# Optimization experiments

Measured on AMD Instinct MI355X. Metric: run time of the kernel, lower is better.

## Reference

```python
import jax, jax.numpy as jnp
import numpy as np

# ---- static hash-grid config (matches tcnn HashGrid in __init__) ----
L = 16            # n_levels
T = 1 << 19       # hashmap size per level
BASE = 16
MAXR = 4096
GEO = 15
SCALE = np.exp((np.log(MAXR) - np.log(BASE)) / (L - 1))
RES = np.floor(BASE * SCALE ** np.arange(L)).astype(np.int64)  # per-level resolution
PRIMES = np.array([1, 2654435761, 805459861], dtype=np.uint32)
CORNERS = np.array([[(i >> 2) & 1, (i >> 1) & 1, i & 1] for i in range(8)], dtype=np.float32)  # [8,3]


@jax.custom_vjp
def trunc_exp(x):
    return jnp.exp(x)

def _te_fwd(x):
    return jnp.exp(x), x

def _te_bwd(x, g):
    return (g * jnp.exp(jnp.minimum(x, 15.0)),)

trunc_exp.defvjp(_te_fwd, _te_bwd)


def hash_encode(x, tables):
    """Multi-res hash grid. x: [N,3] in [0,1]; tables: [L,T,2] -> [N, 2*L]."""
    x = jnp.clip(x, 0.0, 1.0)
    feats = []
    for l in range(L):  # fixed small loop over levels
        res = float(RES[l])
        pos = x * res                      # [N,3]
        p0 = jnp.floor(pos)
        f = pos - p0                       # trilinear fractions
        idx = (p0[:, None, :] + CORNERS[None]).astype(jnp.uint32)  # [N,8,3]
        h = (idx[..., 0] * PRIMES[0]) ^ (idx[..., 1] * PRIMES[1]) ^ (idx[..., 2] * PRIMES[2])
        h = (h % np.uint32(T)).astype(jnp.int32)                   # [N,8]
        w = jnp.prod(jnp.where(CORNERS[None] > 0, f[:, None, :], 1.0 - f[:, None, :]), axis=-1)  # [N,8]
        feats.append(jnp.sum(tables[l][h] * w[..., None], axis=1))  # [N,2]
    return jnp.concatenate(feats, axis=-1)  # [N,32]


def sh_deg4(d):
    """Spherical harmonics degree 4 (16 comps) on unit directions d: [N,3]."""
    x, y, z = d[..., 0], d[..., 1], d[..., 2]
    x2, y2, z2 = x * x, y * y, z * z
    xy, yz, xz = x * y, y * z, x * z
    return jnp.stack([
        jnp.full_like(x, 0.28209479177387814),
        -0.48860251190291987 * y, 0.48860251190291987 * z, -0.48860251190291987 * x,
        1.0925484305920792 * xy, -1.0925484305920792 * yz,
        0.94617469575755997 * z2 - 0.31539156525252005,
        -1.0925484305920792 * xz, 0.54627421529603959 * (x2 - y2),
        -0.5900435899266435 * y * (3 * x2 - y2), 2.890611442640554 * xy * z,
        -0.4570457994644658 * y * (4 * z2 - x2 - y2),
        0.3731763325901154 * z * (2 * z2 - 3 * x2 - 3 * y2),
        -0.4570457994644658 * x * (4 * z2 - x2 - y2),
        1.445305721320277 * z * (x2 - y2),
        -0.5900435899266435 * x * (x2 - 3 * y2),
    ], axis=-1)


def setup_inputs() -> dict:
    key = jax.random.key(0)
    ks = jax.random.split(key, 12)
    R, N = 8192, 524288
    rays_o = jax.random.uniform(ks[0], (R, 3), minval=-0.4, maxval=0.4, dtype=jnp.float32)
    d = jax.random.normal(ks[1], (R, 3), dtype=jnp.float32)
    rays_d = d / jnp.linalg.norm(d, axis=-1, keepdims=True)
    ray_indices = jnp.sort(jax.random.randint(ks[2], (N,), 0, R)).astype(jnp.int32)
    t_starts = jax.random.uniform(ks[3], (N,), dtype=jnp.float32) * 0.25
    t_ends = t_starts + jax.random.uniform(ks[4], (N,), dtype=jnp.float32) * 0.02 + 1e-3
    hash_tables = jax.random.uniform(ks[5], (L, T, 2), minval=-1e-4, maxval=1e-4, dtype=jnp.float32)
    base_w0 = jax.random.normal(ks[6], (32, 64), dtype=jnp.float32) * (1.0 / np.sqrt(32))
    base_w1 = jax.random.normal(ks[7], (64, 16), dtype=jnp.float32) * (1.0 / np.sqrt(64))
    head_w0 = jax.random.normal(ks[8], (31, 64), dtype=jnp.float32) * (1.0 / np.sqrt(31))
    head_w1 = jax.random.normal(ks[9], (64, 64), dtype=jnp.float32) * (1.0 / np.sqrt(64))
    head_w2 = jax.random.normal(ks[10], (64, 3), dtype=jnp.float32) * (1.0 / np.sqrt(64))
    aabb = jnp.array([-1., -1., -1., 1., 1., 1.], dtype=jnp.float32)
    return dict(t_starts=t_starts, t_ends=t_ends, rays_o=rays_o, rays_d=rays_d,
                ray_indices=ray_indices, hash_tables=hash_tables,
                base_w0=base_w0, base_w1=base_w1,
                head_w0=head_w0, head_w1=head_w1, head_w2=head_w2, aabb=aabb)


def reference(t_starts, t_ends, rays_o, rays_d, ray_indices, hash_tables,
              base_w0, base_w1, head_w0, head_w1, head_w2, aabb):
    n_rays = rays_o.shape[0]
    aabb_min, aabb_max = aabb[:3], aabb[3:]
    # gather per-sample origins/dirs (irregular gather)
    t_origins = rays_o[ray_indices]
    t_dirs = rays_d[ray_indices]
    tmid = (t_starts + t_ends) * 0.5
    positions = t_origins + t_dirs * tmid[:, None]
    # query_density
    xn = (positions - aabb_min) / (aabb_max - aabb_min + 1e-5)
    selector = jnp.all((xn > 0.0) & (xn < 1.0), axis=-1)
    enc = hash_encode(xn, hash_tables)                   # [N,32]
    h = jax.nn.relu(enc @ base_w0) @ base_w1             # [N,16]
    sigmas = trunc_exp(h[:, 0] - 1.0) * selector         # [N]
    embedding = h[:, 1:]                                 # [N,15]
    # query_rgb: dir=(dir+1)/2 then SH enc maps back to [-1,1] => SH(t_dirs)
    hh = jnp.concatenate([sh_deg4(t_dirs), embedding], axis=-1)  # [N,31]
    rgbs = jax.nn.sigmoid(jax.nn.relu(jax.nn.relu(hh @ head_w0) @ head_w1) @ head_w2)  # [N,3]
    # render_weight_from_density: segment-wise exclusive transmittance
    s = sigmas * (t_ends - t_starts)
    excl = jnp.cumsum(s) - s                              # global exclusive cumsum
    offsets = jax.ops.segment_min(excl, ray_indices, num_segments=n_rays)  # value at each segment start
    trans = jnp.exp(-(excl - offsets[ray_indices]))
    alphas = 1.0 - jnp.exp(-s)
    weights = trans * alphas
    # accumulate_along_rays (segment_sum scatter)
    colors = jax.ops.segment_sum(weights[:, None] * rgbs, ray_indices, num_segments=n_rays)
    opacities = jax.ops.segment_sum(weights, ray_indices, num_segments=n_rays)[:, None]
    depths = jax.ops.segment_sum(weights * tmid, ray_indices, num_segments=n_rays)[:, None]
    depths = depths / jnp.maximum(opacities, jnp.finfo(jnp.float32).eps)  # expected_depths
    return colors, opacities, depths
```

## Files before the change

kernel.cpp:

```cpp
#include <hip/hip_runtime.h>
#include <math.h>

#define NLEV 16
#define TBL  (1u << 19)
#define TMASK (TBL - 1u)

typedef _Float16 half2v  __attribute__((ext_vector_type(2)));
typedef _Float16 half4   __attribute__((ext_vector_type(4)));
typedef _Float16 half8   __attribute__((ext_vector_type(8)));
typedef float    floatx4 __attribute__((ext_vector_type(4)));
typedef unsigned int uint2v __attribute__((ext_vector_type(2)));
typedef unsigned int uint4v __attribute__((ext_vector_type(4)));

struct ResParams { float resf[NLEV]; };

__device__ __forceinline__ float sigmoidf(float x) {
    return 1.0f / (1.0f + __expf(-x));
}

__device__ __forceinline__ float2 unpack_h2(unsigned u) {
    union { unsigned u; half2v h; } c; c.u = u;
    return make_float2((float)c.h[0], (float)c.h[1]);
}

__device__ __forceinline__ int swz64(int row, int col) {
    return row * 64 + ((((col >> 3) ^ (row & 7)) << 3) | (col & 7));
}
__device__ __forceinline__ int swz64_blk(int row, int blk) {
    return row * 64 + ((blk ^ (row & 7)) << 3);
}
__device__ __forceinline__ int swz16(int row, int col) {
    return row * 64 + ((((col >> 3) ^ (row & 7)) << 3) | (col & 7));
}
__device__ __forceinline__ int swz16_blk(int row, int blk) {
    return row * 64 + ((blk ^ (row & 7)) << 3);
}

__global__ __launch_bounds__(256) void k_cvt(
    const float* __restrict__ src, _Float16* __restrict__ dst, int n4)
{
    const int i = blockIdx.x * 256 + threadIdx.x;
    if (i >= n4) return;
    const float4 v = ((const float4*)src)[i];
    half4 o; o[0] = (_Float16)v.x; o[1] = (_Float16)v.y;
    o[2] = (_Float16)v.z; o[3] = (_Float16)v.w;
    ((half4*)dst)[i] = o;
}

struct SampPos { float x0, x1, x2; };

__device__ __forceinline__ SampPos load_pos(
    int i, const float* __restrict__ t_starts, const float* __restrict__ t_ends,
    const float* __restrict__ rays_o, const float* __restrict__ rays_d,
    const int* __restrict__ ray_indices,
    float a0, float a1, float a2, float ib0, float ib1, float ib2)
{
    const int   ri = ray_indices[i];
    const float tmid = 0.5f * (t_starts[i] + t_ends[i]);
    const float xn0 = (rays_o[ri*3+0] + rays_d[ri*3+0]*tmid - a0) * ib0;
    const float xn1 = (rays_o[ri*3+1] + rays_d[ri*3+1]*tmid - a1) * ib1;
    const float xn2 = (rays_o[ri*3+2] + rays_d[ri*3+2]*tmid - a2) * ib2;
    SampPos p;
    p.x0 = fminf(fmaxf(xn0, 0.f), 1.f);
    p.x1 = fminf(fmaxf(xn1, 0.f), 1.f);
    p.x2 = fminf(fmaxf(xn2, 0.f), 1.f);
    return p;
}

__global__ __launch_bounds__(256) void k_hash1(
    const float* __restrict__ t_starts, const float* __restrict__ t_ends,
    const float* __restrict__ rays_o,   const float* __restrict__ rays_d,
    const int*   __restrict__ ray_indices,
    const _Float16* __restrict__ tabh,
    const float* __restrict__ aabb,
    _Float16* __restrict__ encG, int n, ResParams rp)
{
    const int i = blockIdx.x * 256 + threadIdx.x;
    if (i >= n) return;

    const float a0 = aabb[0], a1 = aabb[1], a2 = aabb[2];
    const float ib0 = 1.f / (aabb[3] - a0 + 1e-5f);
    const float ib1 = 1.f / (aabb[4] - a1 + 1e-5f);
    const float ib2 = 1.f / (aabb[5] - a2 + 1e-5f);

    const SampPos A = load_pos(i, t_starts, t_ends, rays_o, rays_d, ray_indices,
                               a0, a1, a2, ib0, ib1, ib2);

    union { _Float16 h[32]; uint4v q[4]; } ev;

    #pragma unroll
    for (int l = 0; l < NLEV; ++l) {
        const float resf = rp.resf[l];
        const _Float16* __restrict__ tab = tabh + (size_t)l * (size_t)(TBL * 2u);

        const float p0 = A.x0*resf, p1 = A.x1*resf, p2 = A.x2*resf;
        const float fl0 = floorf(p0), fl1 = floorf(p1), fl2 = floorf(p2);
        const float f0 = p0-fl0, f1 = p1-fl1, f2 = p2-fl2;
        const unsigned i0 = (unsigned)fl0, i1 = (unsigned)fl1, i2 = (unsigned)fl2;
        const unsigned hy0 = i1 * 2654435761u, hy1 = hy0 + 2654435761u;
        const unsigned hz0 = i2 * 805459861u,  hz1 = hz0 + 805459861u;
        const float g0 = 1.f-f0, g1 = 1.f-f1, g2 = 1.f-f2;
        const unsigned ryz[4] = { hy0^hz0, hy0^hz1, hy1^hz0, hy1^hz1 };
        const float    wyz[4] = { g1*g2,   g1*f2,   f1*g2,   f1*f2 };

        unsigned v0[4], v1[4];
        if (!(i0 & 1u)) {
            #pragma unroll
            for (int c = 0; c < 4; ++c) {
                const unsigned lo = (i0 ^ ryz[c]) & TMASK;
                const uint2v p = *(const uint2v*)(tab + (size_t)(lo & ~1u) * 2u);
                const unsigned sw = lo & 1u;
                v0[c] = sw ? p.y : p.x;
                v1[c] = sw ? p.x : p.y;
            }
        } else {
            #pragma unroll
            for (int c = 0; c < 4; ++c) {
                const unsigned lo = (i0        ^ ryz[c]) & TMASK;
                const unsigned hi = ((i0 + 1u) ^ ryz[c]) & TMASK;
                v0[c] = *(const unsigned*)(tab + (size_t)lo * 2u);
                v1[c] = *(const unsigned*)(tab + (size_t)hi * 2u);
            }
        }

        float e0 = 0.f, e1 = 0.f;
        #pragma unroll
        for (int c = 0; c < 4; ++c) {
            const float wlo = g0 * wyz[c], whi = f0 * wyz[c];
            const float2 t0 = unpack_h2(v0[c]), t1 = unpack_h2(v1[c]);
            e0 += wlo * t0.x + whi * t1.x;
            e1 += wlo * t0.y + whi * t1.y;
        }
        ev.h[2*l]   = (_Float16)(e0 * 1024.f);
        ev.h[2*l+1] = (_Float16)(e1 * 1024.f);
    }

    uint4v* dst = (uint4v*)(encG + (size_t)i * 32);
    #pragma unroll
    for (int q = 0; q < 4; ++q) __builtin_nontemporal_store(ev.q[q], dst + q);
}

__global__ __launch_bounds__(256) void k_bounds(
    const int* __restrict__ ray_indices, int* __restrict__ se, int n)
{
    const int i = blockIdx.x * 256 + threadIdx.x;
    if (i >= n) return;
    const int r = ray_indices[i];
    if (i == 0 || ray_indices[i-1] != r) se[2*r]     = i;
    if (i == n-1 || ray_indices[i+1] != r) se[2*r+1] = i + 1;
}

__global__ __launch_bounds__(256) void k_mlp(
    const float* __restrict__ t_starts, const float* __restrict__ t_ends,
    const float* __restrict__ rays_o,   const float* __restrict__ rays_d,
    const int*   __restrict__ ray_indices,
    const float* __restrict__ bw0,
    const float* __restrict__ bw1,
    const float* __restrict__ hw0,
    const float* __restrict__ hw1,
    const float* __restrict__ hw2,
    const float* __restrict__ aabb,
    const _Float16* __restrict__ encG,
    float4* __restrict__ srgb, int n)
{
    __shared__ _Float16 sT  [4][2048];
    __shared__ _Float16 sSH [256 * 16];
    __shared__ _Float16 sHB [256 * 16];
    __shared__ _Float16 sW0T[64 * 40];
    __shared__ _Float16 sW1T[64 * 64];
    __shared__ _Float16 sBW0T[64 * 32];
    __shared__ _Float16 sBW1T[16 * 64];
    __shared__ float    sDT [256];

    const int t     = threadIdx.x;
    const int gbase = blockIdx.x * 256;

    {
        const int s  = gbase + t;
        const int ri = ray_indices[s];
        const float ts = t_starts[s], te = t_ends[s];
        const float tmid = 0.5f * (ts + te);
        const float ox = rays_o[ri*3+0], oy = rays_o[ri*3+1], oz = rays_o[ri*3+2];
        const float dx = rays_d[ri*3+0], dy = rays_d[ri*3+1], dz = rays_d[ri*3+2];
        const float a0 = aabb[0], a1 = aabb[1], a2c = aabb[2];
        const float b0 = aabb[3], b1 = aabb[4], b2c = aabb[5];
        const float xn0 = (ox + dx*tmid - a0) / (b0 - a0 + 1e-5f);
        const float xn1 = (oy + dy*tmid - a1) / (b1 - a1 + 1e-5f);
        const float xn2 = (oz + dz*tmid - a2c) / (b2c - a2c + 1e-5f);
        const bool sel = (xn0 > 0.f) && (xn0 < 1.f) && (xn1 > 0.f) && (xn1 < 1.f)
                      && (xn2 > 0.f) && (xn2 < 1.f);
        sDT[t] = sel ? (te - ts) : 0.f;

        const float x = dx, y = dy, z = dz;
        const float x2 = x*x, y2 = y*y, z2 = z*z;
        const float xy = x*y, yz = y*z, xz = x*z;
        float shv[16];
        shv[0]  = 0.28209479177387814f;
        shv[1]  = -0.48860251190291987f * y;
        shv[2]  = 0.48860251190291987f * z;
        shv[3]  = -0.48860251190291987f * x;
        shv[4]  = 1.0925484305920792f * xy;
        shv[5]  = -1.0925484305920792f * yz;
        shv[6]  = 0.94617469575756f * z2 - 0.31539156525252005f;
        shv[7]  = -1.0925484305920792f * xz;
        shv[8]  = 0.5462742152960396f * (x2 - y2);
        shv[9]  = -0.5900435899266435f * y * (3.f*x2 - y2);
        shv[10] = 2.890611442640554f * xy * z;
        shv[11] = -0.4570457994644658f * y * (4.f*z2 - x2 - y2);
        shv[12] = 0.3731763325901154f * z * (2.f*z2 - 3.f*x2 - 3.f*y2);
        shv[13] = -0.4570457994644658f * x * (4.f*z2 - x2 - y2);
        shv[14] = 1.445305721320277f * z * (x2 - y2);
        shv[15] = -0.5900435899266435f * x * (x2 - 3.f*y2);
        #pragma unroll
        for (int k4 = 0; k4 < 4; ++k4) {
            half4 p;
            #pragma unroll
            for (int j = 0; j < 4; ++j) p[j] = (_Float16)shv[k4*4 + j];
            *(half4*)&sSH[t*16 + k4*4] = p;
        }
    }
    {
        const int nidx = t & 63, g = t >> 6;
        #pragma unroll
        for (int i2 = 0; i2 < 8; ++i2) {
            const int k = g*8 + i2;
            const float v = (k < 31) ? hw0[k*64 + nidx] : 0.f;
            sW0T[nidx*40 + k] = (_Float16)v;
        }
        #pragma unroll
        for (int i2 = 0; i2 < 16; ++i2) {
            const int k = g*16 + i2;
            sW1T[swz64(nidx, k)] = (_Float16)hw1[k*64 + nidx];
        }
        #pragma unroll
        for (int i2 = 0; i2 < 8; ++i2) {
            const int k = g*8 + i2;
            sBW0T[nidx*32 + k] = (_Float16)bw0[k*64 + nidx];
        }
    }
    {
        const int nidx = t & 15, g = t >> 4;
        #pragma unroll
        for (int i2 = 0; i2 < 4; ++i2) {
            const int k = g*4 + i2;
            sBW1T[swz16(nidx, k)] = (_Float16)bw1[k*16 + nidx];
        }
    }

    const int lane = t & 63, w = t >> 6;
    const int nn = lane & 15, quad = lane >> 4;
    _Float16* T0 = &sT[w][0];
    _Float16* T1 = &sT[w][1024];

    half8 BH2[2];
    #pragma unroll
    for (int ks = 0; ks < 2; ++ks)
        #pragma unroll
        for (int j = 0; j < 8; ++j) {
            const int k = ks*32 + quad*8 + j;
            BH2[ks][j] = (nn < 3) ? (_Float16)hw2[k*3 + nn] : (_Float16)0.f;
        }

    __syncthreads();

    const int rbase = w * 64;

    #pragma unroll
    for (int p = 0; p < 2; ++p) {
        const int s0 = rbase + p*32;
        const int s1 = s0 + 16;
        const int d0 = s0 + quad*4;
        const int d1 = s1 + quad*4;

        half8 bE0 = *(const half8*)(encG + (size_t)(gbase + s0 + nn)*32 + quad*8);
        half8 bE1 = *(const half8*)(encG + (size_t)(gbase + s1 + nn)*32 + quad*8);
        #pragma unroll
        for (int ct = 0; ct < 4; ++ct) {
            half8 aW = *(const half8*)&sBW0T[(ct*16 + nn)*32 + quad*8];
            floatx4 a0 = {0.f,0.f,0.f,0.f}, a1 = {0.f,0.f,0.f,0.f};
            a0 = __builtin_amdgcn_mfma_f32_16x16x32_f16(aW, bE0, a0, 0, 0, 0);
            a1 = __builtin_amdgcn_mfma_f32_16x16x32_f16(aW, bE1, a1, 0, 0, 0);
            half4 p0, p1;
            #pragma unroll
            for (int r2 = 0; r2 < 4; ++r2) {
                p0[r2] = (_Float16)fmaxf(a0[r2], 0.f);
                p1[r2] = (_Float16)fmaxf(a1[r2], 0.f);
            }
            *(half4*)&T0[swz16(nn, ct*16 + quad*4)] = p0;
            *(half4*)&T1[swz16(nn, ct*16 + quad*4)] = p1;
        }

        float sig0[4], sig1[4];
        {
            half8 b20 = *(const half8*)&sBW1T[swz16_blk(nn, quad)];
            half8 b21 = *(const half8*)&sBW1T[swz16_blk(nn, 4 + quad)];
            half8 a200 = *(const half8*)&T0[swz16_blk(nn, quad)];
            half8 a201 = *(const half8*)&T0[swz16_blk(nn, 4 + quad)];
            half8 a210 = *(const half8*)&T1[swz16_blk(nn, quad)];
            half8 a211 = *(const half8*)&T1[swz16_blk(nn, 4 + quad)];
            floatx4 c0 = {0.f,0.f,0.f,0.f}, c1 = {0.f,0.f,0.f,0.f};
            c0 = __builtin_amdgcn_mfma_f32_16x16x32_f16(a200, b20, c0, 0, 0, 0);
            c1 = __builtin_amdgcn_mfma_f32_16x16x32_f16(a210, b20, c1, 0, 0, 0);
            c0 = __builtin_amdgcn_mfma_f32_16x16x32_f16(a201, b21, c0, 0, 0, 0);
            c1 = __builtin_amdgcn_mfma_f32_16x16x32_f16(a211, b21, c1, 0, 0, 0);
            #pragma unroll
            for (int r2 = 0; r2 < 4; ++r2) {
                const float h0v = c0[r2] * (1.f / 1024.f);
                const float h1v = c1[r2] * (1.f / 1024.f);
                const float b0v = __shfl(h0v, lane & 0x30, 64);
                const float b1v = __shfl(h1v, lane & 0x30, 64);
                sig0[r2] = __expf(b0v - 1.f) * sDT[d0 + r2];
                sig1[r2] = __expf(b1v - 1.f) * sDT[d1 + r2];
                if (nn == 0) {
                    sHB[(d0 + r2)*16 + 15] = (_Float16)0.f;
                    sHB[(d1 + r2)*16 + 15] = (_Float16)0.f;
                } else {
                    sHB[(d0 + r2)*16 + (nn - 1)] = (_Float16)h0v;
                    sHB[(d1 + r2)*16 + (nn - 1)] = (_Float16)h1v;
                }
            }
        }

        half8 sh0 = *(const half8*)&sSH[(s0 + nn)*16 + (quad & 1)*8];
        half8 hb0 = *(const half8*)&sHB[(s0 + nn)*16 + (quad & 1)*8];
        half8 sh1 = *(const half8*)&sSH[(s1 + nn)*16 + (quad & 1)*8];
        half8 hb1 = *(const half8*)&sHB[(s1 + nn)*16 + (quad & 1)*8];
        half8 f30 = (quad < 2) ? sh0 : hb0;
        half8 f31 = (quad < 2) ? sh1 : hb1;
        #pragma unroll
        for (int ct = 0; ct < 4; ++ct) {
            half8 aW = *(const half8*)&sW0T[(ct*16 + nn)*40 + quad*8];
            floatx4 a0 = {0.f,0.f,0.f,0.f}, a1 = {0.f,0.f,0.f,0.f};
            a0 = __builtin_amdgcn_mfma_f32_16x16x32_f16(aW, f30, a0, 0, 0, 0);
            a1 = __builtin_amdgcn_mfma_f32_16x16x32_f16(aW, f31, a1, 0, 0, 0);
            half4 p0, p1;
            #pragma unroll
            for (int r2 = 0; r2 < 4; ++r2) {
                p0[r2] = (_Float16)fmaxf(a0[r2], 0.f);
                p1[r2] = (_Float16)fmaxf(a1[r2], 0.f);
            }
            *(half4*)&T0[swz16(nn, ct*16 + quad*4)] = p0;
            *(half4*)&T1[swz16(nn, ct*16 + quad*4)] = p1;
        }

        half8 af00 = *(const half8*)&T0[swz16_blk(nn, quad)];
        half8 af01 = *(const half8*)&T0[swz16_blk(nn, 4 + quad)];
        half8 af10 = *(const half8*)&T1[swz16_blk(nn, quad)];
        half8 af11 = *(const half8*)&T1[swz16_blk(nn, 4 + quad)];
        #pragma unroll
        for (int ct = 0; ct < 4; ++ct) {
            half8 aW0 = *(const half8*)&sW1T[swz64_blk(ct*16 + nn, quad)];
            half8 aW1 = *(const half8*)&sW1T[swz64_blk(ct*16 + nn, 4 + quad)];
            floatx4 a0 = {0.f,0.f,0.f,0.f}, a1 = {0.f,0.f,0.f,0.f};
            a0 = __builtin_amdgcn_mfma_f32_16x16x32_f16(aW0, af00, a0, 0, 0, 0);
            a1 = __builtin_amdgcn_mfma_f32_16x16x32_f16(aW0, af10, a1, 0, 0, 0);
            a0 = __builtin_amdgcn_mfma_f32_16x16x32_f16(aW1, af01, a0, 0, 0, 0);
            a1 = __builtin_amdgcn_mfma_f32_16x16x32_f16(aW1, af11, a1, 0, 0, 0);
            half4 p0, p1;
            #pragma unroll
            for (int r2 = 0; r2 < 4; ++r2) {
                p0[r2] = (_Float16)fmaxf(a0[r2], 0.f);
                p1[r2] = (_Float16)fmaxf(a1[r2], 0.f);
            }
            *(half4*)&T0[swz16(nn, ct*16 + quad*4)] = p0;
            *(half4*)&T1[swz16(nn, ct*16 + quad*4)] = p1;
        }

        {
            half8 a500 = *(const half8*)&T0[swz16_blk(nn, quad)];
            half8 a501 = *(const half8*)&T0[swz16_blk(nn, 4 + quad)];
            half8 a510 = *(const half8*)&T1[swz16_blk(nn, quad)];
            half8 a511 = *(const half8*)&T1[swz16_blk(nn, 4 + quad)];
            floatx4 c0 = {0.f,0.f,0.f,0.f}, c1 = {0.f,0.f,0.f,0.f};
            c0 = __builtin_amdgcn_mfma_f32_16x16x32_f16(a500, BH2[0], c0, 0, 0, 0);
            c1 = __builtin_amdgcn_mfma_f32_16x16x32_f16(a510, BH2[0], c1, 0, 0, 0);
            c0 = __builtin_amdgcn_mfma_f32_16x16x32_f16(a501, BH2[1], c0, 0, 0, 0);
            c1 = __builtin_amdgcn_mfma_f32_16x16x32_f16(a511, BH2[1], c1, 0, 0, 0);
            #pragma unroll
            for (int r2 = 0; r2 < 4; ++r2) {
                float* bp0 = (float*)&srgb[gbase + d0 + r2];
                float* bp1 = (float*)&srgb[gbase + d1 + r2];
                if (nn < 3) {
                    bp0[1 + nn] = sigmoidf(c0[r2]);
                    bp1[1 + nn] = sigmoidf(c1[r2]);
                } else if (nn == 3) {
                    bp0[0] = sig0[r2];
                    bp1[0] = sig1[r2];
                }
            }
        }
    }
}

__global__ __launch_bounds__(256) void k_render(
    const float* __restrict__ t_starts, const float* __restrict__ t_ends,
    const int*   __restrict__ se,
    const float4* __restrict__ srgb,
    float* __restrict__ out, int n_rays)
{
    const int wid  = (blockIdx.x * 256 + threadIdx.x) >> 6;
    const int lane = threadIdx.x & 63;
    if (wid >= n_rays) return;
    const int r = wid;

    const int start = se[2*r];
    const int end   = se[2*r + 1];

    float S = 0.f, cr = 0.f, cg = 0.f, cb = 0.f, op = 0.f, dw = 0.f;
    for (int j0 = start; j0 < end; j0 += 64) {
        const int j = j0 + lane;
        float s = 0.f, R = 0.f, G = 0.f, B = 0.f, tm = 0.f;
        if (j < end) {
            const float4 v = srgb[j];
            s = v.x; R = v.y; G = v.z; B = v.w;
            tm = 0.5f * (t_starts[j] + t_ends[j]);
        }
        float incl = s;
        #pragma unroll
        for (int off = 1; off < 64; off <<= 1) {
            const float tv = __shfl_up(incl, off, 64);
            if (lane >= off) incl += tv;
        }
        const float excl  = incl - s;
        const float trans = __expf(-(S + excl));
        const float alpha = 1.f - __expf(-s);
        const float wgt   = trans * alpha;
        cr += wgt * R; cg += wgt * G; cb += wgt * B;
        op += wgt;     dw += wgt * tm;
        S += __shfl(incl, 63, 64);
    }
    #pragma unroll
    for (int off = 1; off < 64; off <<= 1) {
        cr += __shfl_xor(cr, off, 64);
        cg += __shfl_xor(cg, off, 64);
        cb += __shfl_xor(cb, off, 64);
        op += __shfl_xor(op, off, 64);
        dw += __shfl_xor(dw, off, 64);
    }
    if (lane == 0) {
        out[r*3 + 0] = cr;
        out[r*3 + 1] = cg;
        out[r*3 + 2] = cb;
        out[n_rays*3 + r] = op;
        out[n_rays*4 + r] = dw / fmaxf(op, 1.1920929e-7f);
    }
}

extern "C" void kernel_launch(void* const* d_in, const int* in_sizes, int n_in,
                              void* d_out, int out_size, void* d_ws, size_t ws_size,
                              hipStream_t stream)
{
    const float* t_starts    = (const float*)d_in[0];
    const float* t_ends      = (const float*)d_in[1];
    const float* rays_o      = (const float*)d_in[2];
    const float* rays_d      = (const float*)d_in[3];
    const int*   ray_indices = (const int*)  d_in[4];
    const float* tables      = (const float*)d_in[5];
    const float* bw0         = (const float*)d_in[6];
    const float* bw1         = (const float*)d_in[7];
    const float* hw0         = (const float*)d_in[8];
    const float* hw1         = (const float*)d_in[9];
    const float* hw2         = (const float*)d_in[10];
    const float* aabb        = (const float*)d_in[11];

    const int n      = in_sizes[0];
    const int n_rays = in_sizes[2] / 3;
    const int tbl_n  = in_sizes[5];

    float* out = (float*)d_out;
    char*  ws  = (char*)d_ws;

    const size_t tabh_bytes = (size_t)tbl_n * 2;
    const size_t enc_bytes  = (size_t)n * 64;
    const size_t srgb_bytes = (size_t)n * 16;

    ResParams rp;
    const double scale = exp((log(4096.0) - log(16.0)) / 15.0);
    for (int l = 0; l < NLEV; ++l)
        rp.resf[l] = (float)floor(16.0 * pow(scale, (double)l));

    _Float16* tabh = (_Float16*)ws;
    _Float16* encG = (_Float16*)(ws + tabh_bytes);
    float4*   srgb = (float4*)(ws + tabh_bytes + enc_bytes);
    int*      se   = (int*)(ws + tabh_bytes + enc_bytes + srgb_bytes);

    const int n4 = tbl_n / 4;
    k_cvt<<<(n4 + 255)/256, 256, 0, stream>>>(tables, tabh, n4);

    hipMemsetAsync(se, 0, (size_t)n_rays * 2 * sizeof(int), stream);
    k_bounds<<<(n + 255)/256, 256, 0, stream>>>(ray_indices, se, n);

    k_hash1<<<(n + 255)/256, 256, 0, stream>>>(
        t_starts, t_ends, rays_o, rays_d, ray_indices, tabh, aabb, encG, n, rp);

    k_mlp<<<(n + 255)/256, 256, 0, stream>>>(
        t_starts, t_ends, rays_o, rays_d, ray_indices, bw0, bw1, hw0, hw1, hw2,
        aabb, encG, srgb, n);

    k_render<<<(n_rays*64 + 255)/256, 256, 0, stream>>>(
        t_starts, t_ends, se, srgb, out, n_rays);
}
```

Baseline: 312.9 us.

## Fuse hash-grid encoding into MLP kernel, computing features directly in MFMA fragments

Removes the separate hash-encoding kernel and its fp16 feature buffer in global memory. Each lane now computes the four hash levels matching its quad for the four sample rows it feeds to the first MFMA, writing results straight into the B-operand registers. This drops a global write and read of 64 bytes per sample and one launch. In exchange, the MLP kernel carries the gather latency and extra register pressure, which may lower occupancy, and the ray position is recomputed per lane.

```diff
diff --git a/kernel.cpp b/kernel.cpp
--- a/kernel.cpp
+++ b/kernel.cpp
@@ -47,99 +47,6 @@
     ((half4*)dst)[i] = o;
 }
 
-struct SampPos { float x0, x1, x2; };
-
-__device__ __forceinline__ SampPos load_pos(
-    int i, const float* __restrict__ t_starts, const float* __restrict__ t_ends,
-    const float* __restrict__ rays_o, const float* __restrict__ rays_d,
-    const int* __restrict__ ray_indices,
-    float a0, float a1, float a2, float ib0, float ib1, float ib2)
-{
-    const int   ri = ray_indices[i];
-    const float tmid = 0.5f * (t_starts[i] + t_ends[i]);
-    const float xn0 = (rays_o[ri*3+0] + rays_d[ri*3+0]*tmid - a0) * ib0;
-    const float xn1 = (rays_o[ri*3+1] + rays_d[ri*3+1]*tmid - a1) * ib1;
-    const float xn2 = (rays_o[ri*3+2] + rays_d[ri*3+2]*tmid - a2) * ib2;
-    SampPos p;
-    p.x0 = fminf(fmaxf(xn0, 0.f), 1.f);
-    p.x1 = fminf(fmaxf(xn1, 0.f), 1.f);
-    p.x2 = fminf(fmaxf(xn2, 0.f), 1.f);
-    return p;
-}
-
-__global__ __launch_bounds__(256) void k_hash1(
-    const float* __restrict__ t_starts, const float* __restrict__ t_ends,
-    const float* __restrict__ rays_o,   const float* __restrict__ rays_d,
-    const int*   __restrict__ ray_indices,
-    const _Float16* __restrict__ tabh,
-    const float* __restrict__ aabb,
-    _Float16* __restrict__ encG, int n, ResParams rp)
-{
-    const int i = blockIdx.x * 256 + threadIdx.x;
-    if (i >= n) return;
-
-    const float a0 = aabb[0], a1 = aabb[1], a2 = aabb[2];
-    const float ib0 = 1.f / (aabb[3] - a0 + 1e-5f);
-    const float ib1 = 1.f / (aabb[4] - a1 + 1e-5f);
-    const float ib2 = 1.f / (aabb[5] - a2 + 1e-5f);
-
-    const SampPos A = load_pos(i, t_starts, t_ends, rays_o, rays_d, ray_indices,
-                               a0, a1, a2, ib0, ib1, ib2);
-
-    union { _Float16 h[32]; uint4v q[4]; } ev;
-
-    #pragma unroll
-    for (int l = 0; l < NLEV; ++l) {
-        const float resf = rp.resf[l];
-        const _Float16* __restrict__ tab = tabh + (size_t)l * (size_t)(TBL * 2u);
-
-        const float p0 = A.x0*resf, p1 = A.x1*resf, p2 = A.x2*resf;
-        const float fl0 = floorf(p0), fl1 = floorf(p1), fl2 = floorf(p2);
-        const float f0 = p0-fl0, f1 = p1-fl1, f2 = p2-fl2;
-        const unsigned i0 = (unsigned)fl0, i1 = (unsigned)fl1, i2 = (unsigned)fl2;
-        const unsigned hy0 = i1 * 2654435761u, hy1 = hy0 + 2654435761u;
-        const unsigned hz0 = i2 * 805459861u,  hz1 = hz0 + 805459861u;
-        const float g0 = 1.f-f0, g1 = 1.f-f1, g2 = 1.f-f2;
-        const unsigned ryz[4] = { hy0^hz0, hy0^hz1, hy1^hz0, hy1^hz1 };
-        const float    wyz[4] = { g1*g2,   g1*f2,   f1*g2,   f1*f2 };
-
-        unsigned v0[4], v1[4];
-        if (!(i0 & 1u)) {
-            #pragma unroll
-            for (int c = 0; c < 4; ++c) {
-                const unsigned lo = (i0 ^ ryz[c]) & TMASK;
-                const uint2v p = *(const uint2v*)(tab + (size_t)(lo & ~1u) * 2u);
-                const unsigned sw = lo & 1u;
-                v0[c] = sw ? p.y : p.x;
-                v1[c] = sw ? p.x : p.y;
-            }
-        } else {
-            #pragma unroll
-            for (int c = 0; c < 4; ++c) {
-                const unsigned lo = (i0        ^ ryz[c]) & TMASK;
-                const unsigned hi = ((i0 + 1u) ^ ryz[c]) & TMASK;
-                v0[c] = *(const unsigned*)(tab + (size_t)lo * 2u);
-                v1[c] = *(const unsigned*)(tab + (size_t)hi * 2u);
-            }
-        }
-
-        float e0 = 0.f, e1 = 0.f;
-        #pragma unroll
-        for (int c = 0; c < 4; ++c) {
-            const float wlo = g0 * wyz[c], whi = f0 * wyz[c];
-            const float2 t0 = unpack_h2(v0[c]), t1 = unpack_h2(v1[c]);
-            e0 += wlo * t0.x + whi * t1.x;
-            e1 += wlo * t0.y + whi * t1.y;
-        }
-        ev.h[2*l]   = (_Float16)(e0 * 1024.f);
-        ev.h[2*l+1] = (_Float16)(e1 * 1024.f);
-    }
-
-    uint4v* dst = (uint4v*)(encG + (size_t)i * 32);
-    #pragma unroll
-    for (int q = 0; q < 4; ++q) __builtin_nontemporal_store(ev.q[q], dst + q);
-}
-
 __global__ __launch_bounds__(256) void k_bounds(
     const int* __restrict__ ray_indices, int* __restrict__ se, int n)
 {
@@ -150,18 +57,18 @@
     if (i == n-1 || ray_indices[i+1] != r) se[2*r+1] = i + 1;
 }
 
-__global__ __launch_bounds__(256) void k_mlp(
+__global__ __launch_bounds__(256) void k_fused(
     const float* __restrict__ t_starts, const float* __restrict__ t_ends,
     const float* __restrict__ rays_o,   const float* __restrict__ rays_d,
     const int*   __restrict__ ray_indices,
+    const _Float16* __restrict__ tabh,
     const float* __restrict__ bw0,
     const float* __restrict__ bw1,
     const float* __restrict__ hw0,
     const float* __restrict__ hw1,
     const float* __restrict__ hw2,
     const float* __restrict__ aabb,
-    const _Float16* __restrict__ encG,
-    float4* __restrict__ srgb, int n)
+    float4* __restrict__ srgb, int n, ResParams rp)
 {
     __shared__ _Float16 sT  [4][2048];
     __shared__ _Float16 sSH [256 * 16];
@@ -171,22 +78,26 @@
     __shared__ _Float16 sBW0T[64 * 32];
     __shared__ _Float16 sBW1T[16 * 64];
     __shared__ float    sDT [256];
+    __shared__ float    sRES[16];
 
     const int t     = threadIdx.x;
     const int gbase = blockIdx.x * 256;
 
+    const float a0 = aabb[0], a1 = aabb[1], a2c = aabb[2];
+    const float ib0 = 1.f / (aabb[3] - a0  + 1e-5f);
+    const float ib1 = 1.f / (aabb[4] - a1  + 1e-5f);
+    const float ib2 = 1.f / (aabb[5] - a2c + 1e-5f);
+
+    if (t < 16) sRES[t] = rp.resf[t];
     {
         const int s  = gbase + t;
         const int ri = ray_indices[s];
         const float ts = t_starts[s], te = t_ends[s];
         const float tmid = 0.5f * (ts + te);
-        const float ox = rays_o[ri*3+0], oy = rays_o[ri*3+1], oz = rays_o[ri*3+2];
         const float dx = rays_d[ri*3+0], dy = rays_d[ri*3+1], dz = rays_d[ri*3+2];
-        const float a0 = aabb[0], a1 = aabb[1], a2c = aabb[2];
-        const float b0 = aabb[3], b1 = aabb[4], b2c = aabb[5];
-        const float xn0 = (ox + dx*tmid - a0) / (b0 - a0 + 1e-5f);
-        const float xn1 = (oy + dy*tmid - a1) / (b1 - a1 + 1e-5f);
-        const float xn2 = (oz + dz*tmid - a2c) / (b2c - a2c + 1e-5f);
+        const float xn0 = (rays_o[ri*3+0] + dx*tmid - a0)  * ib0;
+        const float xn1 = (rays_o[ri*3+1] + dy*tmid - a1)  * ib1;
+        const float xn2 = (rays_o[ri*3+2] + dz*tmid - a2c) * ib2;
         const bool sel = (xn0 > 0.f) && (xn0 < 1.f) && (xn1 > 0.f) && (xn1 < 1.f)
                       && (xn2 > 0.f) && (xn2 < 1.f);
         sDT[t] = sel ? (te - ts) : 0.f;
@@ -249,6 +160,7 @@
 
     const int lane = t & 63, w = t >> 6;
     const int nn = lane & 15, quad = lane >> 4;
+    const int rbase = w * 64;
     _Float16* T0 = &sT[w][0];
     _Float16* T1 = &sT[w][1024];
 
@@ -263,7 +175,67 @@
 
     __syncthreads();
 
-    const int rbase = w * 64;
+    half8 bF[4];
+    #pragma unroll
+    for (int j = 0; j < 4; ++j) {
+        const int s  = gbase + rbase + j*16 + nn;
+        const int ri = ray_indices[s];
+        const float tmid = 0.5f * (t_starts[s] + t_ends[s]);
+        const float xn0 = (rays_o[ri*3+0] + rays_d[ri*3+0]*tmid - a0)  * ib0;
+        const float xn1 = (rays_o[ri*3+1] + rays_d[ri*3+1]*tmid - a1)  * ib1;
+        const float xn2 = (rays_o[ri*3+2] + rays_d[ri*3+2]*tmid - a2c) * ib2;
+        const float x0 = fminf(fmaxf(xn0, 0.f), 1.f);
+        const float x1 = fminf(fmaxf(xn1, 0.f), 1.f);
+        const float x2 = fminf(fmaxf(xn2, 0.f), 1.f);
+
+        #pragma unroll
+        for (int il = 0; il < 4; ++il) {
+            const int l = quad*4 + il;
+            const float resf = sRES[l];
+            const _Float16* __restrict__ tab = tabh + (size_t)l * (size_t)(TBL * 2u);
+
+            const float p0 = x0*resf, p1 = x1*resf, p2 = x2*resf;
+            const float fl0 = floorf(p0), fl1 = floorf(p1), fl2 = floorf(p2);
+            const float f0 = p0-fl0, f1 = p1-fl1, f2 = p2-fl2;
+            const unsigned i0 = (unsigned)fl0, i1 = (unsigned)fl1, i2 = (unsigned)fl2;
+            const unsigned hy0 = i1 * 2654435761u, hy1 = hy0 + 2654435761u;
+            const unsigned hz0 = i2 * 805459861u,  hz1 = hz0 + 805459861u;
+            const float g0 = 1.f-f0, g1 = 1.f-f1, g2 = 1.f-f2;
+            const unsigned ryz[4] = { hy0^hz0, hy0^hz1, hy1^hz0, hy1^hz1 };
+            const float    wyz[4] = { g1*g2,   g1*f2,   f1*g2,   f1*f2 };
+
+            unsigned v0[4], v1[4];
+            if (!(i0 & 1u)) {
+                #pragma unroll
+                for (int c = 0; c < 4; ++c) {
+                    const unsigned lo = (i0 ^ ryz[c]) & TMASK;
+                    const uint2v p = *(const uint2v*)(tab + (size_t)(lo & ~1u) * 2u);
+                    const unsigned sw = lo & 1u;
+                    v0[c] = sw ? p.y : p.x;
+                    v1[c] = sw ? p.x : p.y;
+                }
+            } else {
+                #pragma unroll
+                for (int c = 0; c < 4; ++c) {
+                    const unsigned lo = (i0        ^ ryz[c]) & TMASK;
+                    const unsigned hi = ((i0 + 1u) ^ ryz[c]) & TMASK;
+                    v0[c] = *(const unsigned*)(tab + (size_t)lo * 2u);
+                    v1[c] = *(const unsigned*)(tab + (size_t)hi * 2u);
+                }
+            }
+
+            float e0 = 0.f, e1 = 0.f;
+            #pragma unroll
+            for (int c = 0; c < 4; ++c) {
+                const float wlo = g0 * wyz[c], whi = f0 * wyz[c];
+                const float2 t0 = unpack_h2(v0[c]), t1 = unpack_h2(v1[c]);
+                e0 += wlo * t0.x + whi * t1.x;
+                e1 += wlo * t0.y + whi * t1.y;
+            }
+            bF[j][il*2]     = (_Float16)(e0 * 1024.f);
+            bF[j][il*2 + 1] = (_Float16)(e1 * 1024.f);
+        }
+    }
 
     #pragma unroll
     for (int p = 0; p < 2; ++p) {
@@ -272,19 +244,19 @@
         const int d0 = s0 + quad*4;
         const int d1 = s1 + quad*4;
 
-        half8 bE0 = *(const half8*)(encG + (size_t)(gbase + s0 + nn)*32 + quad*8);
-        half8 bE1 = *(const half8*)(encG + (size_t)(gbase + s1 + nn)*32 + quad*8);
+        half8 bE0 = bF[2*p];
+        half8 bE1 = bF[2*p + 1];
         #pragma unroll
         for (int ct = 0; ct < 4; ++ct) {
             half8 aW = *(const half8*)&sBW0T[(ct*16 + nn)*32 + quad*8];
-            floatx4 a0 = {0.f,0.f,0.f,0.f}, a1 = {0.f,0.f,0.f,0.f};
-            a0 = __builtin_amdgcn_mfma_f32_16x16x32_f16(aW, bE0, a0, 0, 0, 0);
-            a1 = __builtin_amdgcn_mfma_f32_16x16x32_f16(aW, bE1, a1, 0, 0, 0);
+            floatx4 a0v = {0.f,0.f,0.f,0.f}, a1v = {0.f,0.f,0.f,0.f};
+            a0v = __builtin_amdgcn_mfma_f32_16x16x32_f16(aW, bE0, a0v, 0, 0, 0);
+            a1v = __builtin_amdgcn_mfma_f32_16x16x32_f16(aW, bE1, a1v, 0, 0, 0);
             half4 p0, p1;
             #pragma unroll
             for (int r2 = 0; r2 < 4; ++r2) {
-                p0[r2] = (_Float16)fmaxf(a0[r2], 0.f);
-                p1[r2] = (_Float16)fmaxf(a1[r2], 0.f);
+                p0[r2] = (_Float16)fmaxf(a0v[r2], 0.f);
+                p1[r2] = (_Float16)fmaxf(a1v[r2], 0.f);
             }
             *(half4*)&T0[swz16(nn, ct*16 + quad*4)] = p0;
             *(half4*)&T1[swz16(nn, ct*16 + quad*4)] = p1;
@@ -330,14 +302,14 @@
         #pragma unroll
         for (int ct = 0; ct < 4; ++ct) {
             half8 aW = *(const half8*)&sW0T[(ct*16 + nn)*40 + quad*8];
-            floatx4 a0 = {0.f,0.f,0.f,0.f}, a1 = {0.f,0.f,0.f,0.f};
-            a0 = __builtin_amdgcn_mfma_f32_16x16x32_f16(aW, f30, a0, 0, 0, 0);
-            a1 = __builtin_amdgcn_mfma_f32_16x16x32_f16(aW, f31, a1, 0, 0, 0);
+            floatx4 a0v = {0.f,0.f,0.f,0.f}, a1v = {0.f,0.f,0.f,0.f};
+            a0v = __builtin_amdgcn_mfma_f32_16x16x32_f16(aW, f30, a0v, 0, 0, 0);
+            a1v = __builtin_amdgcn_mfma_f32_16x16x32_f16(aW, f31, a1v, 0, 0, 0);
             half4 p0, p1;
             #pragma unroll
             for (int r2 = 0; r2 < 4; ++r2) {
-                p0[r2] = (_Float16)fmaxf(a0[r2], 0.f);
-                p1[r2] = (_Float16)fmaxf(a1[r2], 0.f);
+                p0[r2] = (_Float16)fmaxf(a0v[r2], 0.f);
+                p1[r2] = (_Float16)fmaxf(a1v[r2], 0.f);
             }
             *(half4*)&T0[swz16(nn, ct*16 + quad*4)] = p0;
             *(half4*)&T1[swz16(nn, ct*16 + quad*4)] = p1;
@@ -351,16 +323,16 @@
         for (int ct = 0; ct < 4; ++ct) {
             half8 aW0 = *(const half8*)&sW1T[swz64_blk(ct*16 + nn, quad)];
             half8 aW1 = *(const half8*)&sW1T[swz64_blk(ct*16 + nn, 4 + quad)];
-            floatx4 a0 = {0.f,0.f,0.f,0.f}, a1 = {0.f,0.f,0.f,0.f};
-            a0 = __builtin_amdgcn_mfma_f32_16x16x32_f16(aW0, af00, a0, 0, 0, 0);
-            a1 = __builtin_amdgcn_mfma_f32_16x16x32_f16(aW0, af10, a1, 0, 0, 0);
-            a0 = __builtin_amdgcn_mfma_f32_16x16x32_f16(aW1, af01, a0, 0, 0, 0);
-            a1 = __builtin_amdgcn_mfma_f32_16x16x32_f16(aW1, af11, a1, 0, 0, 0);
+            floatx4 a0v = {0.f,0.f,0.f,0.f}, a1v = {0.f,0.f,0.f,0.f};
+            a0v = __builtin_amdgcn_mfma_f32_16x16x32_f16(aW0, af00, a0v, 0, 0, 0);
+            a1v = __builtin_amdgcn_mfma_f32_16x16x32_f16(aW0, af10, a1v, 0, 0, 0);
+            a0v = __builtin_amdgcn_mfma_f32_16x16x32_f16(aW1, af01, a0v, 0, 0, 0);
+            a1v = __builtin_amdgcn_mfma_f32_16x16x32_f16(aW1, af11, a1v, 0, 0, 0);
             half4 p0, p1;
             #pragma unroll
             for (int r2 = 0; r2 < 4; ++r2) {
-                p0[r2] = (_Float16)fmaxf(a0[r2], 0.f);
-                p1[r2] = (_Float16)fmaxf(a1[r2], 0.f);
+                p0[r2] = (_Float16)fmaxf(a0v[r2], 0.f);
+                p1[r2] = (_Float16)fmaxf(a1v[r2], 0.f);
             }
             *(half4*)&T0[swz16(nn, ct*16 + quad*4)] = p0;
             *(half4*)&T1[swz16(nn, ct*16 + quad*4)] = p1;
@@ -471,7 +443,6 @@
     char*  ws  = (char*)d_ws;
 
     const size_t tabh_bytes = (size_t)tbl_n * 2;
-    const size_t enc_bytes  = (size_t)n * 64;
     const size_t srgb_bytes = (size_t)n * 16;
 
     ResParams rp;
@@ -480,9 +451,8 @@
         rp.resf[l] = (float)floor(16.0 * pow(scale, (double)l));
 
     _Float16* tabh = (_Float16*)ws;
-    _Float16* encG = (_Float16*)(ws + tabh_bytes);
-    float4*   srgb = (float4*)(ws + tabh_bytes + enc_bytes);
-    int*      se   = (int*)(ws + tabh_bytes + enc_bytes + srgb_bytes);
+    float4*   srgb = (float4*)(ws + tabh_bytes);
+    int*      se   = (int*)(ws + tabh_bytes + srgb_bytes);
 
     const int n4 = tbl_n / 4;
     k_cvt<<<(n4 + 255)/256, 256, 0, stream>>>(tables, tabh, n4);
@@ -490,12 +460,9 @@
     hipMemsetAsync(se, 0, (size_t)n_rays * 2 * sizeof(int), stream);
     k_bounds<<<(n + 255)/256, 256, 0, stream>>>(ray_indices, se, n);
 
-    k_hash1<<<(n + 255)/256, 256, 0, stream>>>(
-        t_starts, t_ends, rays_o, rays_d, ray_indices, tabh, aabb, encG, n, rp);
-
-    k_mlp<<<(n + 255)/256, 256, 0, stream>>>(
-        t_starts, t_ends, rays_o, rays_d, ray_indices, bw0, bw1, hw0, hw1, hw2,
-        aabb, encG, srgb, n);
+    k_fused<<<(n + 255)/256, 256, 0, stream>>>(
+        t_starts, t_ends, rays_o, rays_d, ray_indices, tabh,
+        bw0, bw1, hw0, hw1, hw2, aabb, srgb, n, rp);
 
     k_render<<<(n_rays*64 + 255)/256, 256, 0, stream>>>(
         t_starts, t_ends, se, srgb, out, n_rays);
```

New measurement: 452.3 us. +44.6%, slower.
